# Performance work log

Measured on AMD Instinct MI355X. Metric: run time of the kernel, lower is better.

The kernel has to match this reference:

```python
import jax, jax.numpy as jnp
import numpy as np

NUM_HEADS = 16

def setup_inputs() -> dict:
    key = jax.random.key(0)
    ks = jax.random.split(key, 5)
    b, n, d = 2, 2048, 1024
    s = 0.02
    return {
        "x": jax.random.normal(ks[0], (b, n, d), jnp.float32),
        "wq": jax.random.normal(ks[1], (d, d), jnp.float32) * s,
        "wk": jax.random.normal(ks[2], (d, d), jnp.float32) * s,
        "wv": jax.random.normal(ks[3], (d, d), jnp.float32) * s,
        "wo": jax.random.normal(ks[4], (d, d), jnp.float32) * s,
        "bo": jnp.zeros((d,), jnp.float32),
    }

def reference(x, wq, wk, wv, wo, bo):
    b, n, c = x.shape
    h = NUM_HEADS
    hd = c // h
    scale = hd ** -0.5
    # qkv projections (qkv_bias=False); torch Linear computes x @ W.T
    def split_heads(t):
        return t.reshape(b, n, h, hd).transpose(0, 2, 1, 3)  # b h n d
    q = split_heads(x @ wq.T)
    k = split_heads(x @ wk.T)
    v = split_heads(x @ wv.T)
    dots = jnp.einsum('bhid,bhjd->bhij', q, k) * scale
    attn = jax.nn.softmax(dots, axis=-1)  # attn_drop=0 -> identity
    out = jnp.einsum('bhij,bhjd->bhid', attn, v)
    out = out.transpose(0, 2, 1, 3).reshape(b, n, c)
    out = out @ wo.T + bo  # proj_drop=0 -> identity
    return out
```

## Files before the change

### kernel.cpp

```cpp
#include <hip/hip_runtime.h>
#include <hip/hip_bf16.h>

typedef float f32x4 __attribute__((ext_vector_type(4)));
typedef short short8 __attribute__((ext_vector_type(8)));
typedef short short4v __attribute__((ext_vector_type(4)));

#define MFMA(a, b, c) __builtin_amdgcn_mfma_f32_16x16x32_bf16((a), (b), (c), 0, 0, 0)

#if __has_builtin(__builtin_amdgcn_exp2f)
#define EXP2(x) __builtin_amdgcn_exp2f(x)
#else
#define EXP2(x) exp2f(x)
#endif

#define B_  2
#define N_  2048
#define C_  1024
#define H_  16
#define HD_ 64
#define M_  (B_ * N_)

#define QSCALE 0.18033688011112042f

typedef const __attribute__((address_space(1))) void* gp_t;
typedef __attribute__((address_space(3))) void* sp_t;
#define GLL16(g, s) __builtin_amdgcn_global_load_lds((gp_t)(const void*)(g), (sp_t)(void*)(s), 16, 0, 0)

__device__ __forceinline__ short f2bf(float f) {
    union { float fv; unsigned u; } v; v.fv = f;
    unsigned r = v.u + 0x7fffu + ((v.u >> 16) & 1u);
    return (short)(r >> 16);
}
__device__ __forceinline__ unsigned pack_rne(float a, float b) {
    return (unsigned)(unsigned short)f2bf(a) | ((unsigned)(unsigned short)f2bf(b) << 16);
}

__global__ __launch_bounds__(256) void convert_kernel(
    const float* __restrict__ x,  const float* __restrict__ wq,
    const float* __restrict__ wk, const float* __restrict__ wv,
    const float* __restrict__ wo, short* __restrict__ dst)
{
    size_t e = ((size_t)blockIdx.x * 256 + threadIdx.x) * 8;
    const float* src; size_t off;
    if (e < 4194304)      { src = x;  off = e; }
    else if (e < 5242880) { src = wq; off = e - 4194304; }
    else if (e < 6291456) { src = wk; off = e - 5242880; }
    else if (e < 7340032) { src = wv; off = e - 6291456; }
    else                  { src = wo; off = e - 7340032; }
    float4 a = *(const float4*)(src + off);
    float4 b = *(const float4*)(src + off + 4);
    short8 s;
    s[0] = f2bf(a.x); s[1] = f2bf(a.y); s[2] = f2bf(a.z); s[3] = f2bf(a.w);
    s[4] = f2bf(b.x); s[5] = f2bf(b.y); s[6] = f2bf(b.z); s[7] = f2bf(b.w);
    *(short8*)(dst + e) = s;
}

__global__ __launch_bounds__(256, 2) void qkv_gemm(
    const short* __restrict__ xb, const short* __restrict__ Wb,
    short* __restrict__ Qb, short* __restrict__ Kb, short* __restrict__ Vt)
{
    const int m0 = blockIdx.x * 128;
    const int n0 = blockIdx.y * 128;
    __shared__ short As0[128 * 64], Bs0[128 * 64];
    __shared__ short As1[128 * 64], Bs1[128 * 64];
    const int tid  = threadIdx.x;
    const int wave = tid >> 6, lane = tid & 63;
    const int quad = lane >> 4, l16 = lane & 15;
    const int wr = (wave >> 1) * 64, wc = (wave & 1) * 64;
    const int sw = l16 & 7;

    const int rS = tid >> 3;
    const int cS = (tid & 7) ^ (rS & 7);
    const short* A_src = xb + (size_t)(m0 + rS) * C_ + cS * 8;
    const short* B_src = Wb + (size_t)(n0 + rS) * C_ + cS * 8;

#define QKV_STAGE(AS, BS, kk) do { \
    _Pragma("unroll") \
    for (int it = 0; it < 4; ++it) { \
        GLL16(A_src + (size_t)(it * 32) * C_ + (kk), &AS[it * 2048 + tid * 8]); \
        GLL16(B_src + (size_t)(it * 32) * C_ + (kk), &BS[it * 2048 + tid * 8]); \
    } } while (0)

#define QKV_COMPUTE(AS, BS) do { \
    short8 af[4][2], bf[4][2]; \
    _Pragma("unroll") \
    for (int mi = 0; mi < 4; ++mi) { \
        int row = (wr + mi * 16 + l16) * 64; \
        af[mi][0] = *(const short8*)&AS[row + ((quad    ) ^ sw) * 8]; \
        af[mi][1] = *(const short8*)&AS[row + ((quad + 4) ^ sw) * 8]; \
    } \
    _Pragma("unroll") \
    for (int ni = 0; ni < 4; ++ni) { \
        int row = (wc + ni * 16 + l16) * 64; \
        bf[ni][0] = *(const short8*)&BS[row + ((quad    ) ^ sw) * 8]; \
        bf[ni][1] = *(const short8*)&BS[row + ((quad + 4) ^ sw) * 8]; \
    } \
    __builtin_amdgcn_s_setprio(1); \
    _Pragma("unroll") \
    for (int k2 = 0; k2 < 2; ++k2) \
    _Pragma("unroll") \
    for (int mi = 0; mi < 4; ++mi) \
    _Pragma("unroll") \
    for (int ni = 0; ni < 4; ++ni) \
        acc[mi][ni] = MFMA(af[mi][k2], bf[ni][k2], acc[mi][ni]); \
    __builtin_amdgcn_s_setprio(0); } while (0)

    f32x4 acc[4][4] = {};

    QKV_STAGE(As0, Bs0, 0);
    __syncthreads();
    for (int t2 = 0; t2 < 8; ++t2) {
        const int kk1 = t2 * 128 + 64;
        QKV_STAGE(As1, Bs1, kk1);
        QKV_COMPUTE(As0, Bs0);
        __syncthreads();
        if (t2 < 7) QKV_STAGE(As0, Bs0, kk1 + 64);
        QKV_COMPUTE(As1, Bs1);
        __syncthreads();
    }
#undef QKV_STAGE
#undef QKV_COMPUTE

    const int which = n0 >> 10;
    const int nb = n0 & 1023;
    #pragma unroll
    for (int mi = 0; mi < 4; ++mi)
    #pragma unroll
    for (int ni = 0; ni < 4; ++ni)
    #pragma unroll
    for (int r = 0; r < 4; ++r) {
        int m  = m0 + wr + mi * 16 + quad * 4 + r;
        int cc = nb + wc + ni * 16 + l16;
        float av = acc[mi][ni][r];
        if (which == 0) av *= QSCALE;
        short bv = f2bf(av);
        int bb = m >> 11, ns = m & (N_ - 1);
        int h = cc >> 6, d = cc & 63;
        size_t bh = (size_t)(bb * H_ + h);
        if (which == 0)      Qb[(bh * N_ + ns) * HD_ + d] = bv;
        else if (which == 1) Kb[(bh * N_ + ns) * HD_ + d] = bv;
        else                 Vt[(bh * HD_ + d) * N_ + ns] = bv;
    }
}

__global__ __launch_bounds__(256, 4) void attn_split(
    const short* __restrict__ Qb, const short* __restrict__ Kb,
    const short* __restrict__ Vt, float* __restrict__ Opart,
    float* __restrict__ lpart)
{
    const int bid = blockIdx.x;
    const int swz = (bid & 7) * 128 + (bid >> 3);
    const int bh = swz >> 5;
    const int i0 = ((swz >> 1) & 15) * 128;
    const int sp = swz & 1;
    __shared__ short Ks[2][64 * 64];
    __shared__ short Vs[2][64 * 64];
    const int tid  = threadIdx.x;
    const int wave = tid >> 6, lane = tid & 63;
    const int quad = lane >> 4, l16 = lane & 15;
    const int sw = l16 & 7;

    const short* Qg = Qb + ((size_t)bh * N_ + i0) * HD_;
    const short* Kg = Kb + (size_t)bh * N_ * HD_;
    const short* Vg = Vt + (size_t)bh * HD_ * N_;

    const int row0 = tid >> 3,  c0 = (tid & 7) ^ (row0 & 7);
    const int row1 = row0 + 32, c1 = (tid & 7) ^ (row1 & 7);
    const short* KgA0 = Kg + (sp * 1024 + row0) * HD_ + c0 * 8;
    const short* KgA1 = Kg + (sp * 1024 + row1) * HD_ + c1 * 8;
    const short* VgA0 = Vg + (size_t)row0 * N_ + sp * 1024 + c0 * 8;
    const short* VgA1 = Vg + (size_t)row1 * N_ + sp * 1024 + c1 * 8;

    short8 qf[2][2];
    #pragma unroll
    for (int s = 0; s < 2; ++s) {
        const short* qrow = Qg + (wave * 32 + s * 16 + l16) * HD_;
        qf[s][0] = *(const short8*)(qrow + quad * 8);
        qf[s][1] = *(const short8*)(qrow + quad * 8 + 32);
    }

    GLL16(KgA0, &Ks[0][tid * 8]);
    GLL16(KgA1, &Ks[0][(tid + 256) * 8]);
    GLL16(VgA0, &Vs[0][tid * 8]);
    GLL16(VgA1, &Vs[0][(tid + 256) * 8]);
    __syncthreads();

    f32x4 o[2][4] = {};
    float lrow[2] = {0.f, 0.f};

    for (int jt = 0; jt < 16; ++jt) {
        const int cur = jt & 1;
        if (jt + 1 < 16) {
            int j1 = (jt + 1) * 64;
            GLL16(KgA0 + (size_t)j1 * HD_, &Ks[cur ^ 1][tid * 8]);
            GLL16(KgA1 + (size_t)j1 * HD_, &Ks[cur ^ 1][(tid + 256) * 8]);
            GLL16(VgA0 + j1, &Vs[cur ^ 1][tid * 8]);
            GLL16(VgA1 + j1, &Vs[cur ^ 1][(tid + 256) * 8]);
        }
        const short* Kc = Ks[cur];
        const short* Vc = Vs[cur];

        #pragma unroll
        for (int half = 0; half < 2; ++half) {
            unsigned pq[2][4];
            #pragma unroll
            for (int nio = 0; nio < 2; ++nio) {
                int ni = half * 2 + nio;
                int krow = (ni * 16 + l16) * 64;
                short8 kf0 = *(const short8*)&Kc[krow + ((quad ^ sw) * 8)];
                short8 kf1 = *(const short8*)&Kc[krow + (((quad + 4) ^ sw) * 8)];
                #pragma unroll
                for (int s = 0; s < 2; ++s) {
                    f32x4 st = {0.f, 0.f, 0.f, 0.f};
                    __builtin_amdgcn_s_setprio(1);
                    st = MFMA(kf0, qf[s][0], st);
                    st = MFMA(kf1, qf[s][1], st);
                    __builtin_amdgcn_s_setprio(0);
                    union { float f; unsigned u; } e0, e1, e2, e3;
                    e0.f = EXP2(st[0]); e1.f = EXP2(st[1]);
                    e2.f = EXP2(st[2]); e3.f = EXP2(st[3]);
                    lrow[s] += (e0.f + e1.f) + (e2.f + e3.f);
                    pq[s][nio * 2]     = __builtin_amdgcn_perm(e1.u, e0.u, 0x07060302u);
                    pq[s][nio * 2 + 1] = __builtin_amdgcn_perm(e3.u, e2.u, 0x07060302u);
                }
            }
            #pragma unroll
            for (int di = 0; di < 4; ++di) {
                int vrow = (di * 16 + l16) * 64;
                int ch1 = (half * 4 +     (quad >> 1)) ^ sw;
                int ch2 = (half * 4 + 2 + (quad >> 1)) ^ sw;
                union { struct { short4v lo, hi; } p; short8 v; } va;
                va.p.lo = *(const short4v*)&Vc[vrow + ch1 * 8 + (quad & 1) * 4];
                va.p.hi = *(const short4v*)&Vc[vrow + ch2 * 8 + (quad & 1) * 4];
                __builtin_amdgcn_s_setprio(1);
                #pragma unroll
                for (int s = 0; s < 2; ++s) {
                    union { unsigned u[4]; short8 v; } pb;
                    pb.u[0] = pq[s][0]; pb.u[1] = pq[s][1];
                    pb.u[2] = pq[s][2]; pb.u[3] = pq[s][3];
                    o[s][di] = MFMA(va.v, pb.v, o[s][di]);
                }
                __builtin_amdgcn_s_setprio(0);
            }
        }
        __syncthreads();
    }

    #pragma unroll
    for (int s = 0; s < 2; ++s) {
        float l = lrow[s];
        l += __shfl_xor(l, 16, 64);
        l += __shfl_xor(l, 32, 64);
        int ig = i0 + wave * 32 + s * 16 + l16;
        float* obase = Opart + ((size_t)(sp * 32 + bh) * N_ + ig) * HD_;
        #pragma unroll
        for (int di = 0; di < 4; ++di)
            *(f32x4*)(obase + di * 16 + quad * 4) = o[s][di];
        if (quad == 0) lpart[sp * 65536 + bh * N_ + ig] = l;
    }
}

__global__ __launch_bounds__(256) void merge_kernel(
    const float* __restrict__ Opart, const float* __restrict__ lpart,
    short* __restrict__ Ob)
{
    int e8 = (blockIdx.x * 256 + threadIdx.x) * 8;
    int bh = e8 >> 17;
    int rem = e8 & 131071;
    int ig = rem >> 6, d = rem & 63;
    f32x4 a0 = *(const f32x4*)(Opart + e8);
    f32x4 a1 = *(const f32x4*)(Opart + e8 + 4);
    f32x4 b0 = *(const f32x4*)(Opart + 4194304 + e8);
    f32x4 b1 = *(const f32x4*)(Opart + 4194304 + e8 + 4);
    float inv = 1.f / (lpart[bh * N_ + ig] + lpart[65536 + bh * N_ + ig]);
    short8 s;
    s[0] = f2bf((a0[0] + b0[0]) * inv); s[1] = f2bf((a0[1] + b0[1]) * inv);
    s[2] = f2bf((a0[2] + b0[2]) * inv); s[3] = f2bf((a0[3] + b0[3]) * inv);
    s[4] = f2bf((a1[0] + b1[0]) * inv); s[5] = f2bf((a1[1] + b1[1]) * inv);
    s[6] = f2bf((a1[2] + b1[2]) * inv); s[7] = f2bf((a1[3] + b1[3]) * inv);
    int b = bh >> 4, h = bh & (H_ - 1);
    *(short8*)&Ob[((size_t)(b * N_ + ig)) * C_ + h * HD_ + d] = s;
}

__global__ __launch_bounds__(256, 2) void proj_gemm(
    const short* __restrict__ Ob, const short* __restrict__ wob,
    const float* __restrict__ bo, float* __restrict__ out)
{
    const int m0 = blockIdx.x * 64;
    const int n0 = blockIdx.y * 128;
    __shared__ short As0[64 * 64], Bs0[128 * 64];
    __shared__ short As1[64 * 64], Bs1[128 * 64];
    const int tid  = threadIdx.x;
    const int wave = tid >> 6, lane = tid & 63;
    const int quad = lane >> 4, l16 = lane & 15;
    const int wr = (wave >> 1) * 32, wc = (wave & 1) * 64;
    const int sw = l16 & 7;

    const int rS = tid >> 3;
    const int cS = (tid & 7) ^ (rS & 7);
    const short* A_src = Ob  + (size_t)(m0 + rS) * C_ + cS * 8;
    const short* B_src = wob + (size_t)(n0 + rS) * C_ + cS * 8;

#define PRJ_STAGE(AS, BS, kk) do { \
    GLL16(A_src + (kk), &AS[tid * 8]); \
    GLL16(A_src + (size_t)32 * C_ + (kk), &AS[(tid + 256) * 8]); \
    _Pragma("unroll") \
    for (int it = 0; it < 4; ++it) \
        GLL16(B_src + (size_t)(it * 32) * C_ + (kk), &BS[it * 2048 + tid * 8]); \
    } while (0)

#define PRJ_COMPUTE(AS, BS) do { \
    short8 af[2][2], bf[4][2]; \
    _Pragma("unroll") \
    for (int mi = 0; mi < 2; ++mi) { \
        int row = (wr + mi * 16 + l16) * 64; \
        af[mi][0] = *(const short8*)&AS[row + ((quad    ) ^ sw) * 8]; \
        af[mi][1] = *(const short8*)&AS[row + ((quad + 4) ^ sw) * 8]; \
    } \
    _Pragma("unroll") \
    for (int ni = 0; ni < 4; ++ni) { \
        int row = (wc + ni * 16 + l16) * 64; \
        bf[ni][0] = *(const short8*)&BS[row + ((quad    ) ^ sw) * 8]; \
        bf[ni][1] = *(const short8*)&BS[row + ((quad + 4) ^ sw) * 8]; \
    } \
    __builtin_amdgcn_s_setprio(1); \
    _Pragma("unroll") \
    for (int k2 = 0; k2 < 2; ++k2) \
    _Pragma("unroll") \
    for (int mi = 0; mi < 2; ++mi) \
    _Pragma("unroll") \
    for (int ni = 0; ni < 4; ++ni) \
        acc[mi][ni] = MFMA(af[mi][k2], bf[ni][k2], acc[mi][ni]); \
    __builtin_amdgcn_s_setprio(0); } while (0)

    f32x4 acc[2][4] = {};

    PRJ_STAGE(As0, Bs0, 0);
    __syncthreads();
    for (int t2 = 0; t2 < 8; ++t2) {
        const int kk1 = t2 * 128 + 64;
        PRJ_STAGE(As1, Bs1, kk1);
        PRJ_COMPUTE(As0, Bs0);
        __syncthreads();
        if (t2 < 7) PRJ_STAGE(As0, Bs0, kk1 + 64);
        PRJ_COMPUTE(As1, Bs1);
        __syncthreads();
    }
#undef PRJ_STAGE
#undef PRJ_COMPUTE

    #pragma unroll
    for (int mi = 0; mi < 2; ++mi)
    #pragma unroll
    for (int ni = 0; ni < 4; ++ni)
    #pragma unroll
    for (int r = 0; r < 4; ++r) {
        int m = m0 + wr + mi * 16 + quad * 4 + r;
        int c = n0 + wc + ni * 16 + l16;
        out[(size_t)m * C_ + c] = acc[mi][ni][r] + bo[c];
    }
}

extern "C" void kernel_launch(void* const* d_in, const int* in_sizes, int n_in,
                              void* d_out, int out_size, void* d_ws, size_t ws_size,
                              hipStream_t stream) {
    const float* x  = (const float*)d_in[0];
    const float* wq = (const float*)d_in[1];
    const float* wk = (const float*)d_in[2];
    const float* wv = (const float*)d_in[3];
    const float* wo = (const float*)d_in[4];
    const float* bo = (const float*)d_in[5];
    float* out = (float*)d_out;

    short* xb  = (short*)d_ws;
    short* Wb  = xb  + 4194304;
    short* wob = Wb  + 3145728;
    short* Qb  = wob + 1048576;
    short* Kb  = Qb  + 4194304;
    short* Vt  = Kb  + 4194304;
    short* Obuf= Vt  + 4194304;
    float* Opart = (float*)(Obuf + 4194304);
    float* lpart = Opart + 2 * 4194304;

    dim3 blk(256);
    convert_kernel<<<4096, blk, 0, stream>>>(x, wq, wk, wv, wo, xb);
    qkv_gemm<<<dim3(M_ / 128, 3072 / 128), blk, 0, stream>>>(xb, Wb, Qb, Kb, Vt);
    attn_split<<<1024, blk, 0, stream>>>(Qb, Kb, Vt, Opart, lpart);
    merge_kernel<<<2048, blk, 0, stream>>>(Opart, lpart, Obuf);
    proj_gemm<<<dim3(M_ / 64, C_ / 128), blk, 0, stream>>>(Obuf, wob, bo, out);
}
```

Baseline: 177.7 us.

## Fuse split-attention merge into output projection GEMM A-tile staging

Removes the separate merge kernel and its bf16 intermediate buffer. The projection GEMM now loads the two fp32 attention partials and the row sums directly, normalizes them, converts to bf16 and writes the A tile into LDS itself. B tiles still use async global-to-LDS loads. This saves a launch and a write/read round trip of the merged output. In exchange, every column block re-reads fp32 partials (twice the bytes of bf16, repeated across the 8 column blocks), and the A loads now go through registers, raising register pressure.

```diff
diff --git a/kernel.cpp b/kernel.cpp
--- a/kernel.cpp
+++ b/kernel.cpp
@@ -30,9 +30,6 @@
     union { float fv; unsigned u; } v; v.fv = f;
     unsigned r = v.u + 0x7fffu + ((v.u >> 16) & 1u);
     return (short)(r >> 16);
-}
-__device__ __forceinline__ unsigned pack_rne(float a, float b) {
-    return (unsigned)(unsigned short)f2bf(a) | ((unsigned)(unsigned short)f2bf(b) << 16);
 }
 
 __global__ __launch_bounds__(256) void convert_kernel(
@@ -260,31 +257,10 @@
     }
 }
 
-__global__ __launch_bounds__(256) void merge_kernel(
+__global__ __launch_bounds__(256, 2) void proj_gemm(
     const float* __restrict__ Opart, const float* __restrict__ lpart,
-    short* __restrict__ Ob)
-{
-    int e8 = (blockIdx.x * 256 + threadIdx.x) * 8;
-    int bh = e8 >> 17;
-    int rem = e8 & 131071;
-    int ig = rem >> 6, d = rem & 63;
-    f32x4 a0 = *(const f32x4*)(Opart + e8);
-    f32x4 a1 = *(const f32x4*)(Opart + e8 + 4);
-    f32x4 b0 = *(const f32x4*)(Opart + 4194304 + e8);
-    f32x4 b1 = *(const f32x4*)(Opart + 4194304 + e8 + 4);
-    float inv = 1.f / (lpart[bh * N_ + ig] + lpart[65536 + bh * N_ + ig]);
-    short8 s;
-    s[0] = f2bf((a0[0] + b0[0]) * inv); s[1] = f2bf((a0[1] + b0[1]) * inv);
-    s[2] = f2bf((a0[2] + b0[2]) * inv); s[3] = f2bf((a0[3] + b0[3]) * inv);
-    s[4] = f2bf((a1[0] + b1[0]) * inv); s[5] = f2bf((a1[1] + b1[1]) * inv);
-    s[6] = f2bf((a1[2] + b1[2]) * inv); s[7] = f2bf((a1[3] + b1[3]) * inv);
-    int b = bh >> 4, h = bh & (H_ - 1);
-    *(short8*)&Ob[((size_t)(b * N_ + ig)) * C_ + h * HD_ + d] = s;
-}
-
-__global__ __launch_bounds__(256, 2) void proj_gemm(
-    const short* __restrict__ Ob, const short* __restrict__ wob,
-    const float* __restrict__ bo, float* __restrict__ out)
+    const short* __restrict__ wob, const float* __restrict__ bo,
+    float* __restrict__ out)
 {
     const int m0 = blockIdx.x * 64;
     const int n0 = blockIdx.y * 128;
@@ -298,16 +274,51 @@
 
     const int rS = tid >> 3;
     const int cS = (tid & 7) ^ (rS & 7);
-    const short* A_src = Ob  + (size_t)(m0 + rS) * C_ + cS * 8;
+    const int bh16 = (m0 >> 11) * 16;
+    const int igr  = m0 & (N_ - 1);
     const short* B_src = wob + (size_t)(n0 + rS) * C_ + cS * 8;
 
-#define PRJ_STAGE(AS, BS, kk) do { \
-    GLL16(A_src + (kk), &AS[tid * 8]); \
-    GLL16(A_src + (size_t)32 * C_ + (kk), &AS[(tid + 256) * 8]); \
+    f32x4 qa0, qa1, qb0, qb1;
+    f32x4 ra0, ra1, rb0, rb1;
+    float lA, lB;
+
+#define PRJ_A_LOAD(kk) do { \
+    int h_ = (kk) >> 6; \
+    const float* p0 = Opart + (size_t)(bh16 + h_) * 131072 \
+                    + (size_t)(igr + rS) * 64 + cS * 8; \
+    qa0 = *(const f32x4*)(p0); \
+    qa1 = *(const f32x4*)(p0 + 4); \
+    qb0 = *(const f32x4*)(p0 + 4194304); \
+    qb1 = *(const f32x4*)(p0 + 4194304 + 4); \
+    ra0 = *(const f32x4*)(p0 + 2048); \
+    ra1 = *(const f32x4*)(p0 + 2048 + 4); \
+    rb0 = *(const f32x4*)(p0 + 4194304 + 2048); \
+    rb1 = *(const f32x4*)(p0 + 4194304 + 2048 + 4); \
+    int lb = (bh16 + h_) * 2048 + igr + rS; \
+    lA = lpart[lb] + lpart[65536 + lb]; \
+    lB = lpart[lb + 32] + lpart[65536 + lb + 32]; \
+} while (0)
+
+#define PRJ_A_WRITE(AS) do { \
+    float ia = 1.f / lA, ib = 1.f / lB; \
+    short8 s0, s1; \
+    s0[0] = f2bf((qa0[0] + qb0[0]) * ia); s0[1] = f2bf((qa0[1] + qb0[1]) * ia); \
+    s0[2] = f2bf((qa0[2] + qb0[2]) * ia); s0[3] = f2bf((qa0[3] + qb0[3]) * ia); \
+    s0[4] = f2bf((qa1[0] + qb1[0]) * ia); s0[5] = f2bf((qa1[1] + qb1[1]) * ia); \
+    s0[6] = f2bf((qa1[2] + qb1[2]) * ia); s0[7] = f2bf((qa1[3] + qb1[3]) * ia); \
+    s1[0] = f2bf((ra0[0] + rb0[0]) * ib); s1[1] = f2bf((ra0[1] + rb0[1]) * ib); \
+    s1[2] = f2bf((ra0[2] + rb0[2]) * ib); s1[3] = f2bf((ra0[3] + rb0[3]) * ib); \
+    s1[4] = f2bf((ra1[0] + rb1[0]) * ib); s1[5] = f2bf((ra1[1] + rb1[1]) * ib); \
+    s1[6] = f2bf((ra1[2] + rb1[2]) * ib); s1[7] = f2bf((ra1[3] + rb1[3]) * ib); \
+    *(short8*)&AS[tid * 8] = s0; \
+    *(short8*)&AS[(tid + 256) * 8] = s1; \
+} while (0)
+
+#define PRJ_B(BS, kk) do { \
     _Pragma("unroll") \
     for (int it = 0; it < 4; ++it) \
         GLL16(B_src + (size_t)(it * 32) * C_ + (kk), &BS[it * 2048 + tid * 8]); \
-    } while (0)
+} while (0)
 
 #define PRJ_COMPUTE(AS, BS) do { \
     short8 af[2][2], bf[4][2]; \
@@ -335,18 +346,25 @@
 
     f32x4 acc[2][4] = {};
 
-    PRJ_STAGE(As0, Bs0, 0);
+    PRJ_A_LOAD(0);
+    PRJ_B(Bs0, 0);
+    PRJ_A_WRITE(As0);
     __syncthreads();
     for (int t2 = 0; t2 < 8; ++t2) {
         const int kk1 = t2 * 128 + 64;
-        PRJ_STAGE(As1, Bs1, kk1);
+        PRJ_A_LOAD(kk1);
+        PRJ_B(Bs1, kk1);
         PRJ_COMPUTE(As0, Bs0);
+        PRJ_A_WRITE(As1);
         __syncthreads();
-        if (t2 < 7) PRJ_STAGE(As0, Bs0, kk1 + 64);
+        if (t2 < 7) { PRJ_A_LOAD(kk1 + 64); PRJ_B(Bs0, kk1 + 64); }
         PRJ_COMPUTE(As1, Bs1);
+        if (t2 < 7) PRJ_A_WRITE(As0);
         __syncthreads();
     }
-#undef PRJ_STAGE
+#undef PRJ_A_LOAD
+#undef PRJ_A_WRITE
+#undef PRJ_B
 #undef PRJ_COMPUTE
 
     #pragma unroll
@@ -386,6 +404,5 @@
     convert_kernel<<<4096, blk, 0, stream>>>(x, wq, wk, wv, wo, xb);
     qkv_gemm<<<dim3(M_ / 128, 3072 / 128), blk, 0, stream>>>(xb, Wb, Qb, Kb, Vt);
     attn_split<<<1024, blk, 0, stream>>>(Qb, Kb, Vt, Opart, lpart);
-    merge_kernel<<<2048, blk, 0, stream>>>(Opart, lpart, Obuf);
-    proj_gemm<<<dim3(M_ / 64, C_ / 128), blk, 0, stream>>>(Obuf, wob, bo, out);
-}
+    proj_gemm<<<dim3(M_ / 64, C_ / 128), blk, 0, stream>>>(Opart, lpart, wob, bo, out);
+}
```

Result: slower. 183.8 us (+3.4%).
